# Optimization experiments

Measured on AMD Instinct MI355X. Metric: run time of the kernel, lower is better.

Reference implementation:

```python
import jax, jax.numpy as jnp
import numpy as np

N_NODES = 100000


def _sage_conv(x, edge_index, W_n, W_s, b):
    # edge_index: [2, E] with row0 = src, row1 = dst (messages flow src -> dst)
    src, dst = edge_index[0], edge_index[1]
    msgs = x[src]                                   # [E, F] gather
    summed = jax.ops.segment_sum(msgs, dst, num_segments=N_NODES)   # [N, F]
    deg = jax.ops.segment_sum(jnp.ones((edge_index.shape[1],), x.dtype), dst,
                              num_segments=N_NODES)                 # [N]
    mean = summed / jnp.maximum(deg, 1.0)[:, None]  # mean aggregation
    return mean @ W_n + x @ W_s + b


def setup_inputs() -> dict:
    key = jax.random.key(0)
    ks = jax.random.split(key, 8)
    in_dim, hid_dim, out_dim = 64, 64, 32
    n_edges = 1600000
    x = jax.random.normal(ks[0], (N_NODES, in_dim), dtype=jnp.float32)
    edge_index = jax.random.randint(ks[1], (2, n_edges), 0, N_NODES, dtype=jnp.int64)
    s1 = 1.0 / np.sqrt(in_dim)
    s2 = 1.0 / np.sqrt(hid_dim)
    W1_n = jax.random.uniform(ks[2], (in_dim, hid_dim), jnp.float32, -s1, s1)
    W1_s = jax.random.uniform(ks[3], (in_dim, hid_dim), jnp.float32, -s1, s1)
    b1 = jnp.zeros((hid_dim,), jnp.float32)
    W2_n = jax.random.uniform(ks[4], (hid_dim, out_dim), jnp.float32, -s2, s2)
    W2_s = jax.random.uniform(ks[5], (hid_dim, out_dim), jnp.float32, -s2, s2)
    b2 = jnp.zeros((out_dim,), jnp.float32)
    return {"x": x, "edge_index": edge_index, "W1_n": W1_n, "W1_s": W1_s,
            "b1": b1, "W2_n": W2_n, "W2_s": W2_s, "b2": b2}


def reference(x, edge_index, W1_n, W1_s, b1, W2_n, W2_s, b2):
    h = _sage_conv(x, edge_index, W1_n, W1_s, b1)
    h = jax.nn.relu(h)
    # dropout(p=0.5) is identity in eval mode
    out = _sage_conv(h, edge_index, W2_n, W2_s, b2)
    return out
```

## Files before the change

### kernel.cpp

```cpp
#include <hip/hip_runtime.h>
#include <hip/hip_bf16.h>

#define N_NODES 100000
#define NB 784
#define NPAD 100352
#define BSH 7
#define BMASK 127
#define CAP 4096
#define MSTRIDE 36

typedef float v2f __attribute__((ext_vector_type(2)));

__device__ inline void fma4(float a, const float4& w, float4& c) {
  c.x = fmaf(a, w.x, c.x);
  c.y = fmaf(a, w.y, c.y);
  c.z = fmaf(a, w.z, c.z);
  c.w = fmaf(a, w.w, c.w);
}
__device__ inline unsigned short f2bf(float f) {
  unsigned u = __float_as_uint(f);
  u += 0x7fffu + ((u >> 16) & 1u);
  return (unsigned short)(u >> 16);
}
__device__ inline unsigned pack2bf(float a, float b) {
  return (unsigned)f2bf(a) | ((unsigned)f2bf(b) << 16);
}
__device__ inline unsigned packfp8x4(float a, float b, float c, float d) {
  int pk = __builtin_amdgcn_cvt_pk_fp8_f32(a, b, 0, false);
  pk = __builtin_amdgcn_cvt_pk_fp8_f32(c, d, pk, true);
  return (unsigned)pk;
}
__device__ inline float4 relu_mix(uint2 m, uint2 s) {
  float4 v;
  v.x = fmaxf(__uint_as_float(m.x << 16) + __uint_as_float(s.x << 16), 0.f);
  v.y = fmaxf(__uint_as_float(m.x & 0xffff0000u) +
                  __uint_as_float(s.x & 0xffff0000u), 0.f);
  v.z = fmaxf(__uint_as_float(m.y << 16) + __uint_as_float(s.y << 16), 0.f);
  v.w = fmaxf(__uint_as_float(m.y & 0xffff0000u) +
                  __uint_as_float(s.y & 0xffff0000u), 0.f);
  return v;
}
__device__ inline void acc16(const uint4& u, float* acc) {
  v2f f0 = __builtin_amdgcn_cvt_pk_f32_fp8((int)u.x, false);
  v2f f1 = __builtin_amdgcn_cvt_pk_f32_fp8((int)u.x, true);
  v2f f2 = __builtin_amdgcn_cvt_pk_f32_fp8((int)u.y, false);
  v2f f3 = __builtin_amdgcn_cvt_pk_f32_fp8((int)u.y, true);
  v2f f4 = __builtin_amdgcn_cvt_pk_f32_fp8((int)u.z, false);
  v2f f5 = __builtin_amdgcn_cvt_pk_f32_fp8((int)u.z, true);
  v2f f6 = __builtin_amdgcn_cvt_pk_f32_fp8((int)u.w, false);
  v2f f7 = __builtin_amdgcn_cvt_pk_f32_fp8((int)u.w, true);
  acc[0] += f0[0];  acc[1] += f0[1];
  acc[2] += f1[0];  acc[3] += f1[1];
  acc[4] += f2[0];  acc[5] += f2[1];
  acc[6] += f3[0];  acc[7] += f3[1];
  acc[8] += f4[0];  acc[9] += f4[1];
  acc[10] += f5[0]; acc[11] += f5[1];
  acc[12] += f6[0]; acc[13] += f6[1];
  acc[14] += f7[0]; acc[15] += f7[1];
}

#define EPB 8192
#define EPT 32
#define GB1 1563

__global__ __launch_bounds__(256) void fusedA_k(
    const int* __restrict__ src, const int* __restrict__ dst,
    unsigned* __restrict__ bcur, unsigned* __restrict__ ep,
    const float* __restrict__ x, const float* __restrict__ W1n,
    const float* __restrict__ W1s, const float* __restrict__ b1,
    unsigned* __restrict__ xnb8, unsigned short* __restrict__ xsb,
    int E, int NSB, int M) {
  __shared__ __align__(16) float smem[8192];
  const int tid = threadIdx.x;

  if ((int)blockIdx.x < NSB) {
    unsigned* lh = (unsigned*)smem;
    unsigned* lbase = lh + NB;
    for (int i = tid; i < NB; i += 256) lh[i] = 0;
    __syncthreads();
    const int ebase = blockIdx.x * EPB;
    unsigned rb[EPT];
#pragma unroll
    for (int it = 0; it < EPT; ++it) {
      int e = ebase + it * 256 + tid;
      if (e < E) {
        unsigned b = ((unsigned)dst[e]) >> BSH;
        unsigned r = atomicAdd(&lh[b], 1u);
        rb[it] = (r << 10) | b;
      }
    }
    __syncthreads();
    for (int i = tid; i < NB; i += 256)
      lbase[i] = lh[i] ? atomicAdd(&bcur[i], lh[i]) : 0u;
    __syncthreads();
#pragma unroll
    for (int it = 0; it < EPT; ++it) {
      int e = ebase + it * 256 + tid;
      if (e < E) {
        unsigned b = rb[it] & 1023u;
        unsigned r = rb[it] >> 10;
        ep[(size_t)b * CAP + lbase[b] + r] =
            (((unsigned)src[e]) << BSH) | (((unsigned)dst[e]) & BMASK);
      }
    }
    return;
  }

  float* Wn = smem;
  float* Ws = smem + 4096;
  const int row0 = ((int)blockIdx.x - NSB) * 64;

  for (int i = tid; i < 1024; i += 256) {
    ((float4*)Wn)[i] = ((const float4*)W1n)[i];
    ((float4*)Ws)[i] = ((const float4*)W1s)[i];
  }

  const int tx = tid & 15;
  const int ty = tid >> 4;
  const int arow = ty * 4;

  const float* xr[4];
#pragma unroll
  for (int r = 0; r < 4; ++r) {
    long long gr = row0 + arow + r;
    if (gr >= M) gr = M - 1;
    xr[r] = x + gr * 64;
  }

  float4 an[4], as[4];
#pragma unroll
  for (int r = 0; r < 4; ++r) {
    an[r] = make_float4(0.f, 0.f, 0.f, 0.f);
    as[r] = make_float4(0.f, 0.f, 0.f, 0.f);
  }
  __syncthreads();

#pragma unroll 2
  for (int k4 = 0; k4 < 16; ++k4) {
    float4 a[4];
#pragma unroll
    for (int r = 0; r < 4; ++r) a[r] = *(const float4*)(xr[r] + 4 * k4);
    float4 wn0 = *(const float4*)&Wn[(4 * k4 + 0) * 64 + 4 * tx];
    float4 wn1 = *(const float4*)&Wn[(4 * k4 + 1) * 64 + 4 * tx];
    float4 wn2 = *(const float4*)&Wn[(4 * k4 + 2) * 64 + 4 * tx];
    float4 wn3 = *(const float4*)&Wn[(4 * k4 + 3) * 64 + 4 * tx];
    float4 ws0 = *(const float4*)&Ws[(4 * k4 + 0) * 64 + 4 * tx];
    float4 ws1 = *(const float4*)&Ws[(4 * k4 + 1) * 64 + 4 * tx];
    float4 ws2 = *(const float4*)&Ws[(4 * k4 + 2) * 64 + 4 * tx];
    float4 ws3 = *(const float4*)&Ws[(4 * k4 + 3) * 64 + 4 * tx];
#pragma unroll
    for (int r = 0; r < 4; ++r) {
      fma4(a[r].x, wn0, an[r]);
      fma4(a[r].y, wn1, an[r]);
      fma4(a[r].z, wn2, an[r]);
      fma4(a[r].w, wn3, an[r]);
      fma4(a[r].x, ws0, as[r]);
      fma4(a[r].y, ws1, as[r]);
      fma4(a[r].z, ws2, as[r]);
      fma4(a[r].w, ws3, as[r]);
    }
  }

  const float4 bv = *(const float4*)&b1[4 * tx];
#pragma unroll
  for (int r = 0; r < 4; ++r) {
    int row = row0 + arow + r;
    if (row < M) {
      ushort4 ps;
      ps.x = f2bf(as[r].x + bv.x);
      ps.y = f2bf(as[r].y + bv.y);
      ps.z = f2bf(as[r].z + bv.z);
      ps.w = f2bf(as[r].w + bv.w);
      *(ushort4*)&xsb[(long long)row * 64 + 4 * tx] = ps;
      xnb8[(size_t)row * 16 + tx] =
          packfp8x4(an[r].x, an[r].y, an[r].z, an[r].w);
    }
  }
}

__global__ __launch_bounds__(256) void bsort_k(const unsigned* __restrict__ ep,
                                               const unsigned* __restrict__ bcur,
                                               int* __restrict__ ssrc,
                                               uint2* __restrict__ rows2) {
  __shared__ unsigned cnt[128];
  __shared__ unsigned sc[128];
  const int tid = threadIdx.x;
  const int b = blockIdx.x;
  const unsigned cntb = bcur[b];
  const unsigned beg = (unsigned)(b * CAP);
  if (tid < 128) cnt[tid] = 0;
  __syncthreads();
  for (unsigned j = tid; j < cntb; j += 256)
    atomicAdd(&cnt[ep[(size_t)beg + j] & BMASK], 1u);
  __syncthreads();
  unsigned v = (tid < 128) ? cnt[tid] : 0u;
  if (tid < 128) sc[tid] = v;
  __syncthreads();
  for (int off = 1; off < 128; off <<= 1) {
    unsigned t = (tid < 128 && tid >= off) ? sc[tid - off] : 0u;
    __syncthreads();
    if (tid < 128) sc[tid] += t;
    __syncthreads();
  }
  if (tid < 128) {
    unsigned ex = sc[tid] - v;
    rows2[b * 128 + tid] = make_uint2(beg + ex, beg + ex + v);
    cnt[tid] = ex;
  }
  __syncthreads();
  for (unsigned j = tid; j < cntb; j += 256) {
    unsigned p = ep[(size_t)beg + j];
    unsigned r = atomicAdd(&cnt[p & BMASK], 1u);
    ssrc[(size_t)beg + r] = (int)(p >> BSH);
  }
}

__global__ __launch_bounds__(256) void fgg_k(
    const uint4* __restrict__ valb4, const int* __restrict__ ssrc,
    const uint2* __restrict__ rows2, const unsigned short* __restrict__ xsb,
    const float* __restrict__ W2n, const float* __restrict__ W2s,
    const float* __restrict__ b2, unsigned* __restrict__ hnb8,
    float* __restrict__ hs, int M) {
  __shared__ float Wn[64 * 32];
  __shared__ float Ws[64 * 32];
  __shared__ unsigned mlds[64 * MSTRIDE];
  __shared__ unsigned degs[64];
  __shared__ unsigned begs[64];
  __shared__ unsigned char perm[64];
  const int tid = threadIdx.x;
  const int node0 = blockIdx.x * 64;

  for (int i = tid; i < 512; i += 256) {
    ((float4*)Wn)[i] = ((const float4*)W2n)[i];
    ((float4*)Ws)[i] = ((const float4*)W2s)[i];
  }

  if (tid < 64) {
    uint2 be = rows2[node0 + tid];
    degs[tid] = be.y - be.x;
    begs[tid] = be.x;
  }
  __syncthreads();
  if (tid < 64) {
    unsigned d = degs[tid];
    int rank = 0;
    for (int j2 = 0; j2 < 64; ++j2) {
      unsigned dj = degs[j2];
      rank += (dj < d) || (dj == d && j2 < tid);
    }
    perm[rank] = (unsigned char)tid;
  }
  __syncthreads();

  const int slot = tid >> 2;
  const int lrow = perm[slot];
  const int p = tid & 3;
  const unsigned dg = degs[lrow];
  const unsigned beg = begs[lrow];
  const unsigned end = beg + dg;

  float acc[16];
#pragma unroll
  for (int q = 0; q < 16; ++q) acc[q] = 0.f;

  unsigned j = beg;
  for (; j + 8 <= end; j += 8) {
    int sn[8];
#pragma unroll
    for (int i = 0; i < 8; ++i) sn[i] = ssrc[j + i];
    uint4 u[8];
#pragma unroll
    for (int i = 0; i < 8; ++i) u[i] = valb4[(size_t)sn[i] * 4 + p];
#pragma unroll
    for (int i = 0; i < 8; ++i) acc16(u[i], acc);
  }
  if (j < end) {
    uint4 u[8];
#pragma unroll
    for (int i = 0; i < 8; ++i) {
      u[i] = make_uint4(0u, 0u, 0u, 0u);
      if (j + i < end) {
        int s = ssrc[j + i];
        u[i] = valb4[(size_t)s * 4 + p];
      }
    }
#pragma unroll
    for (int i = 0; i < 8; ++i) acc16(u[i], acc);
  }

  const float inv = dg ? 1.f / (float)dg : 0.f;
  uint4 pk0, pk1;
  pk0.x = pack2bf(acc[0] * inv, acc[1] * inv);
  pk0.y = pack2bf(acc[2] * inv, acc[3] * inv);
  pk0.z = pack2bf(acc[4] * inv, acc[5] * inv);
  pk0.w = pack2bf(acc[6] * inv, acc[7] * inv);
  pk1.x = pack2bf(acc[8] * inv, acc[9] * inv);
  pk1.y = pack2bf(acc[10] * inv, acc[11] * inv);
  pk1.z = pack2bf(acc[12] * inv, acc[13] * inv);
  pk1.w = pack2bf(acc[14] * inv, acc[15] * inv);
  *(uint4*)&mlds[lrow * MSTRIDE + p * 8] = pk0;
  *(uint4*)&mlds[lrow * MSTRIDE + p * 8 + 4] = pk1;
  __syncthreads();

  const int tx = tid & 7;
  const int ty = tid >> 3;
  const int arow = ty * 2;

  const uint2* mp[2];
  const uint2* sp[2];
#pragma unroll
  for (int r = 0; r < 2; ++r) {
    long long gr = node0 + arow + r;
    if (gr >= M) gr = M - 1;
    mp[r] = (const uint2*)&mlds[(arow + r) * MSTRIDE];
    sp[r] = (const uint2*)(xsb + gr * 64);
  }

  float4 an[2], as[2];
#pragma unroll
  for (int r = 0; r < 2; ++r) {
    an[r] = make_float4(0.f, 0.f, 0.f, 0.f);
    as[r] = make_float4(0.f, 0.f, 0.f, 0.f);
  }

#pragma unroll 2
  for (int k4 = 0; k4 < 16; ++k4) {
    float4 a[2];
#pragma unroll
    for (int r = 0; r < 2; ++r) a[r] = relu_mix(mp[r][k4], sp[r][k4]);
    float4 wn0 = *(const float4*)&Wn[(4 * k4 + 0) * 32 + 4 * tx];
    float4 wn1 = *(const float4*)&Wn[(4 * k4 + 1) * 32 + 4 * tx];
    float4 wn2 = *(const float4*)&Wn[(4 * k4 + 2) * 32 + 4 * tx];
    float4 wn3 = *(const float4*)&Wn[(4 * k4 + 3) * 32 + 4 * tx];
    float4 ws0 = *(const float4*)&Ws[(4 * k4 + 0) * 32 + 4 * tx];
    float4 ws1 = *(const float4*)&Ws[(4 * k4 + 1) * 32 + 4 * tx];
    float4 ws2 = *(const float4*)&Ws[(4 * k4 + 2) * 32 + 4 * tx];
    float4 ws3 = *(const float4*)&Ws[(4 * k4 + 3) * 32 + 4 * tx];
#pragma unroll
    for (int r = 0; r < 2; ++r) {
      fma4(a[r].x, wn0, an[r]);
      fma4(a[r].y, wn1, an[r]);
      fma4(a[r].z, wn2, an[r]);
      fma4(a[r].w, wn3, an[r]);
      fma4(a[r].x, ws0, as[r]);
      fma4(a[r].y, ws1, as[r]);
      fma4(a[r].z, ws2, as[r]);
      fma4(a[r].w, ws3, as[r]);
    }
  }

  const float4 bv = *(const float4*)&b2[4 * tx];
#pragma unroll
  for (int r = 0; r < 2; ++r) {
    int row = node0 + arow + r;
    if (row < M) {
      float4 o;
      o.x = as[r].x + bv.x;
      o.y = as[r].y + bv.y;
      o.z = as[r].z + bv.z;
      o.w = as[r].w + bv.w;
      *(float4*)&hs[(long long)row * 32 + 4 * tx] = o;
      hnb8[(size_t)row * 8 + tx] =
          packfp8x4(an[r].x, an[r].y, an[r].z, an[r].w);
    }
  }
}

__global__ __launch_bounds__(256) void gather2_k(
    const uint4* __restrict__ valb4, const int* __restrict__ ssrc,
    const uint2* __restrict__ rows2, const float* __restrict__ base,
    float* __restrict__ out, int N) {
  __shared__ unsigned degs[128];
  __shared__ unsigned begs[128];
  __shared__ unsigned char perm[128];
  const int tid = threadIdx.x;
  const int node0 = blockIdx.x * 128;

  if (tid < 128) {
    uint2 be = rows2[node0 + tid];
    degs[tid] = be.y - be.x;
    begs[tid] = be.x;
  }
  __syncthreads();
  if (tid < 128) {
    unsigned d = degs[tid];
    int rank = 0;
    for (int j2 = 0; j2 < 128; ++j2) {
      unsigned dj = degs[j2];
      rank += (dj < d) || (dj == d && j2 < tid);
    }
    perm[rank] = (unsigned char)tid;
  }
  __syncthreads();

  const int slot = tid >> 1;
  const int lrow = perm[slot];
  const int node = node0 + lrow;
  const int p = tid & 1;
  const unsigned dg = degs[lrow];
  const unsigned beg = begs[lrow];
  const unsigned end = beg + dg;

  float acc[16];
#pragma unroll
  for (int q = 0; q < 16; ++q) acc[q] = 0.f;

  unsigned j = beg;
  for (; j + 8 <= end; j += 8) {
    int sn[8];
#pragma unroll
    for (int i = 0; i < 8; ++i) sn[i] = ssrc[j + i];
    uint4 u[8];
#pragma unroll
    for (int i = 0; i < 8; ++i) u[i] = valb4[(size_t)sn[i] * 2 + p];
#pragma unroll
    for (int i = 0; i < 8; ++i) acc16(u[i], acc);
  }
  if (j < end) {
    uint4 u[8];
#pragma unroll
    for (int i = 0; i < 8; ++i) {
      u[i] = make_uint4(0u, 0u, 0u, 0u);
      if (j + i < end) {
        int s = ssrc[j + i];
        u[i] = valb4[(size_t)s * 2 + p];
      }
    }
#pragma unroll
    for (int i = 0; i < 8; ++i) acc16(u[i], acc);
  }

  if (node < N) {
    const float inv = dg ? 1.f / (float)dg : 0.f;
    const size_t o = (size_t)node * 32 + 16 * p;
#pragma unroll
    for (int q4 = 0; q4 < 4; ++q4) {
      float4 bv = *(const float4*)&base[o + 4 * q4];
      float4 ov;
      ov.x = acc[4 * q4 + 0] * inv + bv.x;
      ov.y = acc[4 * q4 + 1] * inv + bv.y;
      ov.z = acc[4 * q4 + 2] * inv + bv.z;
      ov.w = acc[4 * q4 + 3] * inv + bv.w;
      *(float4*)&out[o + 4 * q4] = ov;
    }
  }
}

extern "C" void kernel_launch(void* const* d_in, const int* in_sizes, int n_in,
                              void* d_out, int out_size, void* d_ws,
                              size_t ws_size, hipStream_t stream) {
  const float* x   = (const float*)d_in[0];
  const int*   ei  = (const int*)d_in[1];
  const float* W1n = (const float*)d_in[2];
  const float* W1s = (const float*)d_in[3];
  const float* b1  = (const float*)d_in[4];
  const float* W2n = (const float*)d_in[5];
  const float* W2s = (const float*)d_in[6];
  const float* b2  = (const float*)d_in[7];
  float* out = (float*)d_out;

  const int E = in_sizes[1] / 2;
  const int M = N_NODES;
  const int* src = ei;
  const int* dst = ei + E;
  const int NSB = (E + EPB - 1) / EPB;

  char* wsb = (char*)d_ws;
  unsigned*       ep    = (unsigned*)(wsb);
  int*            ssrc  = (int*)(wsb + 12845056);
  uint2*          rows2 = (uint2*)(wsb + 25690112);
  unsigned*       bcur  = (unsigned*)(wsb + 26492928);
  unsigned*       xnb8  = (unsigned*)(wsb + 26496064);
  unsigned short* xsb   = (unsigned short*)(wsb + 32896064);
  float*          hs    = (float*)(wsb + 45696064);
  unsigned*       hnb8  = (unsigned*)(wsb);

  hipMemsetAsync(bcur, 0, NB * 4, stream);
  fusedA_k<<<NSB + GB1, 256, 0, stream>>>(src, dst, bcur, ep, x, W1n, W1s, b1,
                                          xnb8, xsb, E, NSB, M);
  bsort_k<<<NB, 256, 0, stream>>>(ep, bcur, ssrc, rows2);
  fgg_k<<<GB1, 256, 0, stream>>>((const uint4*)xnb8, ssrc, rows2, xsb, W2n,
                                 W2s, b2, hnb8, hs, M);
  gather2_k<<<(M + 127) / 128, 256, 0, stream>>>((const uint4*)hnb8, ssrc,
                                                 rows2, hs, out, M);
}
```

Before: 216.1 us.

## Split each node's edge range across two threads and drop degree sorting

In both gather kernels, each node's neighbor list is now split in half and given to two threads, whose partial sums are combined with a cross-lane shuffle. This replaces the in-block degree ranking and permutation, which added shared memory, two barriers and O(n^2) rank work. The edge tail now uses clamped unconditional loads with a 0/1 weight instead of branches. Blocks cover fewer nodes (32 in fgg, 64 in gather2), so more blocks run. Without degree sorting, lanes in a wavefront may see more divergence when neighboring nodes have different degrees.

```diff
diff --git a/kernel.cpp b/kernel.cpp
--- a/kernel.cpp
+++ b/kernel.cpp
@@ -8,6 +8,7 @@
 #define BMASK 127
 #define CAP 4096
 #define MSTRIDE 36
+#define FNB 32
 
 typedef float v2f __attribute__((ext_vector_type(2)));
 
@@ -58,6 +59,24 @@
   acc[12] += f6[0]; acc[13] += f6[1];
   acc[14] += f7[0]; acc[15] += f7[1];
 }
+__device__ inline void macc16(const uint4& u, float w, float* acc) {
+  v2f f0 = __builtin_amdgcn_cvt_pk_f32_fp8((int)u.x, false);
+  v2f f1 = __builtin_amdgcn_cvt_pk_f32_fp8((int)u.x, true);
+  v2f f2 = __builtin_amdgcn_cvt_pk_f32_fp8((int)u.y, false);
+  v2f f3 = __builtin_amdgcn_cvt_pk_f32_fp8((int)u.y, true);
+  v2f f4 = __builtin_amdgcn_cvt_pk_f32_fp8((int)u.z, false);
+  v2f f5 = __builtin_amdgcn_cvt_pk_f32_fp8((int)u.z, true);
+  v2f f6 = __builtin_amdgcn_cvt_pk_f32_fp8((int)u.w, false);
+  v2f f7 = __builtin_amdgcn_cvt_pk_f32_fp8((int)u.w, true);
+  acc[0] = fmaf(w, f0[0], acc[0]);   acc[1] = fmaf(w, f0[1], acc[1]);
+  acc[2] = fmaf(w, f1[0], acc[2]);   acc[3] = fmaf(w, f1[1], acc[3]);
+  acc[4] = fmaf(w, f2[0], acc[4]);   acc[5] = fmaf(w, f2[1], acc[5]);
+  acc[6] = fmaf(w, f3[0], acc[6]);   acc[7] = fmaf(w, f3[1], acc[7]);
+  acc[8] = fmaf(w, f4[0], acc[8]);   acc[9] = fmaf(w, f4[1], acc[9]);
+  acc[10] = fmaf(w, f5[0], acc[10]); acc[11] = fmaf(w, f5[1], acc[11]);
+  acc[12] = fmaf(w, f6[0], acc[12]); acc[13] = fmaf(w, f6[1], acc[13]);
+  acc[14] = fmaf(w, f7[0], acc[14]); acc[15] = fmaf(w, f7[1], acc[15]);
+}
 
 #define EPB 8192
 #define EPT 32
@@ -223,48 +242,32 @@
     float* __restrict__ hs, int M) {
   __shared__ float Wn[64 * 32];
   __shared__ float Ws[64 * 32];
-  __shared__ unsigned mlds[64 * MSTRIDE];
-  __shared__ unsigned degs[64];
-  __shared__ unsigned begs[64];
-  __shared__ unsigned char perm[64];
+  __shared__ unsigned mlds[FNB * MSTRIDE];
   const int tid = threadIdx.x;
-  const int node0 = blockIdx.x * 64;
+  const int node0 = blockIdx.x * FNB;
 
   for (int i = tid; i < 512; i += 256) {
     ((float4*)Wn)[i] = ((const float4*)W2n)[i];
     ((float4*)Ws)[i] = ((const float4*)W2s)[i];
   }
 
-  if (tid < 64) {
-    uint2 be = rows2[node0 + tid];
-    degs[tid] = be.y - be.x;
-    begs[tid] = be.x;
-  }
-  __syncthreads();
-  if (tid < 64) {
-    unsigned d = degs[tid];
-    int rank = 0;
-    for (int j2 = 0; j2 < 64; ++j2) {
-      unsigned dj = degs[j2];
-      rank += (dj < d) || (dj == d && j2 < tid);
-    }
-    perm[rank] = (unsigned char)tid;
-  }
-  __syncthreads();
-
-  const int slot = tid >> 2;
-  const int lrow = perm[slot];
-  const int p = tid & 3;
-  const unsigned dg = degs[lrow];
-  const unsigned beg = begs[lrow];
-  const unsigned end = beg + dg;
+  const int lrow = tid >> 3;
+  const int q = tid & 7;
+  const int p = q & 3;
+  const int t = q >> 2;
+  const int node = node0 + lrow;
+  const uint2 be = rows2[node];
+  const unsigned dg = be.y - be.x;
+  const unsigned mid = be.x + ((dg + 1) >> 1);
+  const unsigned tb = t ? mid : be.x;
+  const unsigned te = t ? be.y : mid;
 
   float acc[16];
 #pragma unroll
-  for (int q = 0; q < 16; ++q) acc[q] = 0.f;
-
-  unsigned j = beg;
-  for (; j + 8 <= end; j += 8) {
+  for (int qq = 0; qq < 16; ++qq) acc[qq] = 0.f;
+
+  unsigned j = tb;
+  for (; j + 8 <= te; j += 8) {
     int sn[8];
 #pragma unroll
     for (int i = 0; i < 8; ++i) sn[i] = ssrc[j + i];
@@ -274,60 +277,53 @@
 #pragma unroll
     for (int i = 0; i < 8; ++i) acc16(u[i], acc);
   }
-  if (j < end) {
+  if (j < te) {
+    const unsigned last = te - 1;
+    int sn[8];
+#pragma unroll
+    for (int i = 0; i < 8; ++i) {
+      unsigned jj = j + i;
+      sn[i] = ssrc[jj < last ? jj : last];
+    }
     uint4 u[8];
 #pragma unroll
-    for (int i = 0; i < 8; ++i) {
-      u[i] = make_uint4(0u, 0u, 0u, 0u);
-      if (j + i < end) {
-        int s = ssrc[j + i];
-        u[i] = valb4[(size_t)s * 4 + p];
-      }
-    }
-#pragma unroll
-    for (int i = 0; i < 8; ++i) acc16(u[i], acc);
-  }
+    for (int i = 0; i < 8; ++i) u[i] = valb4[(size_t)sn[i] * 4 + p];
+#pragma unroll
+    for (int i = 0; i < 8; ++i) macc16(u[i], ((j + i) < te) ? 1.f : 0.f, acc);
+  }
+
+#pragma unroll
+  for (int qq = 0; qq < 16; ++qq) acc[qq] += __shfl_xor(acc[qq], 4);
 
   const float inv = dg ? 1.f / (float)dg : 0.f;
-  uint4 pk0, pk1;
-  pk0.x = pack2bf(acc[0] * inv, acc[1] * inv);
-  pk0.y = pack2bf(acc[2] * inv, acc[3] * inv);
-  pk0.z = pack2bf(acc[4] * inv, acc[5] * inv);
-  pk0.w = pack2bf(acc[6] * inv, acc[7] * inv);
-  pk1.x = pack2bf(acc[8] * inv, acc[9] * inv);
-  pk1.y = pack2bf(acc[10] * inv, acc[11] * inv);
-  pk1.z = pack2bf(acc[12] * inv, acc[13] * inv);
-  pk1.w = pack2bf(acc[14] * inv, acc[15] * inv);
-  *(uint4*)&mlds[lrow * MSTRIDE + p * 8] = pk0;
-  *(uint4*)&mlds[lrow * MSTRIDE + p * 8 + 4] = pk1;
+  if (t == 0) {
+    uint4 pk;
+    pk.x = pack2bf(acc[0] * inv, acc[1] * inv);
+    pk.y = pack2bf(acc[2] * inv, acc[3] * inv);
+    pk.z = pack2bf(acc[4] * inv, acc[5] * inv);
+    pk.w = pack2bf(acc[6] * inv, acc[7] * inv);
+    *(uint4*)&mlds[lrow * MSTRIDE + p * 8] = pk;
+  } else {
+    uint4 pk;
+    pk.x = pack2bf(acc[8] * inv, acc[9] * inv);
+    pk.y = pack2bf(acc[10] * inv, acc[11] * inv);
+    pk.z = pack2bf(acc[12] * inv, acc[13] * inv);
+    pk.w = pack2bf(acc[14] * inv, acc[15] * inv);
+    *(uint4*)&mlds[lrow * MSTRIDE + p * 8 + 4] = pk;
+  }
   __syncthreads();
 
   const int tx = tid & 7;
   const int ty = tid >> 3;
-  const int arow = ty * 2;
-
-  const uint2* mp[2];
-  const uint2* sp[2];
-#pragma unroll
-  for (int r = 0; r < 2; ++r) {
-    long long gr = node0 + arow + r;
-    if (gr >= M) gr = M - 1;
-    mp[r] = (const uint2*)&mlds[(arow + r) * MSTRIDE];
-    sp[r] = (const uint2*)(xsb + gr * 64);
-  }
-
-  float4 an[2], as[2];
-#pragma unroll
-  for (int r = 0; r < 2; ++r) {
-    an[r] = make_float4(0.f, 0.f, 0.f, 0.f);
-    as[r] = make_float4(0.f, 0.f, 0.f, 0.f);
-  }
+  const uint2* mp = (const uint2*)&mlds[ty * MSTRIDE];
+  const uint2* sp = (const uint2*)(xsb + (long long)(node0 + ty) * 64);
+
+  float4 an = make_float4(0.f, 0.f, 0.f, 0.f);
+  float4 asv = make_float4(0.f, 0.f, 0.f, 0.f);
 
 #pragma unroll 2
   for (int k4 = 0; k4 < 16; ++k4) {
-    float4 a[2];
-#pragma unroll
-    for (int r = 0; r < 2; ++r) a[r] = relu_mix(mp[r][k4], sp[r][k4]);
+    float4 a = relu_mix(mp[k4], sp[k4]);
     float4 wn0 = *(const float4*)&Wn[(4 * k4 + 0) * 32 + 4 * tx];
     float4 wn1 = *(const float4*)&Wn[(4 * k4 + 1) * 32 + 4 * tx];
     float4 wn2 = *(const float4*)&Wn[(4 * k4 + 2) * 32 + 4 * tx];
@@ -336,77 +332,50 @@
     float4 ws1 = *(const float4*)&Ws[(4 * k4 + 1) * 32 + 4 * tx];
     float4 ws2 = *(const float4*)&Ws[(4 * k4 + 2) * 32 + 4 * tx];
     float4 ws3 = *(const float4*)&Ws[(4 * k4 + 3) * 32 + 4 * tx];
-#pragma unroll
-    for (int r = 0; r < 2; ++r) {
-      fma4(a[r].x, wn0, an[r]);
-      fma4(a[r].y, wn1, an[r]);
-      fma4(a[r].z, wn2, an[r]);
-      fma4(a[r].w, wn3, an[r]);
-      fma4(a[r].x, ws0, as[r]);
-      fma4(a[r].y, ws1, as[r]);
-      fma4(a[r].z, ws2, as[r]);
-      fma4(a[r].w, ws3, as[r]);
-    }
+    fma4(a.x, wn0, an);
+    fma4(a.y, wn1, an);
+    fma4(a.z, wn2, an);
+    fma4(a.w, wn3, an);
+    fma4(a.x, ws0, asv);
+    fma4(a.y, ws1, asv);
+    fma4(a.z, ws2, asv);
+    fma4(a.w, ws3, asv);
   }
 
   const float4 bv = *(const float4*)&b2[4 * tx];
-#pragma unroll
-  for (int r = 0; r < 2; ++r) {
-    int row = node0 + arow + r;
-    if (row < M) {
-      float4 o;
-      o.x = as[r].x + bv.x;
-      o.y = as[r].y + bv.y;
-      o.z = as[r].z + bv.z;
-      o.w = as[r].w + bv.w;
-      *(float4*)&hs[(long long)row * 32 + 4 * tx] = o;
-      hnb8[(size_t)row * 8 + tx] =
-          packfp8x4(an[r].x, an[r].y, an[r].z, an[r].w);
-    }
-  }
+  const int row = node0 + ty;
+  float4 o;
+  o.x = asv.x + bv.x;
+  o.y = asv.y + bv.y;
+  o.z = asv.z + bv.z;
+  o.w = asv.w + bv.w;
+  *(float4*)&hs[(long long)row * 32 + 4 * tx] = o;
+  hnb8[(size_t)row * 8 + tx] = packfp8x4(an.x, an.y, an.z, an.w);
 }
 
 __global__ __launch_bounds__(256) void gather2_k(
     const uint4* __restrict__ valb4, const int* __restrict__ ssrc,
     const uint2* __restrict__ rows2, const float* __restrict__ base,
     float* __restrict__ out, int N) {
-  __shared__ unsigned degs[128];
-  __shared__ unsigned begs[128];
-  __shared__ unsigned char perm[128];
   const int tid = threadIdx.x;
-  const int node0 = blockIdx.x * 128;
-
-  if (tid < 128) {
-    uint2 be = rows2[node0 + tid];
-    degs[tid] = be.y - be.x;
-    begs[tid] = be.x;
-  }
-  __syncthreads();
-  if (tid < 128) {
-    unsigned d = degs[tid];
-    int rank = 0;
-    for (int j2 = 0; j2 < 128; ++j2) {
-      unsigned dj = degs[j2];
-      rank += (dj < d) || (dj == d && j2 < tid);
-    }
-    perm[rank] = (unsigned char)tid;
-  }
-  __syncthreads();
-
-  const int slot = tid >> 1;
-  const int lrow = perm[slot];
+  const int node0 = blockIdx.x * 64;
+  const int lrow = tid >> 2;
+  const int q = tid & 3;
+  const int p = q & 1;
+  const int t = q >> 1;
   const int node = node0 + lrow;
-  const int p = tid & 1;
-  const unsigned dg = degs[lrow];
-  const unsigned beg = begs[lrow];
-  const unsigned end = beg + dg;
+  const uint2 be = rows2[node];
+  const unsigned dg = be.y - be.x;
+  const unsigned mid = be.x + ((dg + 1) >> 1);
+  const unsigned tb = t ? mid : be.x;
+  const unsigned te = t ? be.y : mid;
 
   float acc[16];
 #pragma unroll
-  for (int q = 0; q < 16; ++q) acc[q] = 0.f;
-
-  unsigned j = beg;
-  for (; j + 8 <= end; j += 8) {
+  for (int qq = 0; qq < 16; ++qq) acc[qq] = 0.f;
+
+  unsigned j = tb;
+  for (; j + 8 <= te; j += 8) {
     int sn[8];
 #pragma unroll
     for (int i = 0; i < 8; ++i) sn[i] = ssrc[j + i];
@@ -416,25 +385,30 @@
 #pragma unroll
     for (int i = 0; i < 8; ++i) acc16(u[i], acc);
   }
-  if (j < end) {
+  if (j < te) {
+    const unsigned last = te - 1;
+    int sn[8];
+#pragma unroll
+    for (int i = 0; i < 8; ++i) {
+      unsigned jj = j + i;
+      sn[i] = ssrc[jj < last ? jj : last];
+    }
     uint4 u[8];
 #pragma unroll
-    for (int i = 0; i < 8; ++i) {
-      u[i] = make_uint4(0u, 0u, 0u, 0u);
-      if (j + i < end) {
-        int s = ssrc[j + i];
-        u[i] = valb4[(size_t)s * 2 + p];
-      }
-    }
-#pragma unroll
-    for (int i = 0; i < 8; ++i) acc16(u[i], acc);
-  }
+    for (int i = 0; i < 8; ++i) u[i] = valb4[(size_t)sn[i] * 2 + p];
+#pragma unroll
+    for (int i = 0; i < 8; ++i) macc16(u[i], ((j + i) < te) ? 1.f : 0.f, acc);
+  }
+
+#pragma unroll
+  for (int qq = 0; qq < 16; ++qq) acc[qq] += __shfl_xor(acc[qq], 2);
 
   if (node < N) {
     const float inv = dg ? 1.f / (float)dg : 0.f;
     const size_t o = (size_t)node * 32 + 16 * p;
 #pragma unroll
-    for (int q4 = 0; q4 < 4; ++q4) {
+    for (int h = 0; h < 2; ++h) {
+      const int q4 = 2 * t + h;
       float4 bv = *(const float4*)&base[o + 4 * q4];
       float4 ov;
       ov.x = acc[4 * q4 + 0] * inv + bv.x;
@@ -479,8 +453,9 @@
   fusedA_k<<<NSB + GB1, 256, 0, stream>>>(src, dst, bcur, ep, x, W1n, W1s, b1,
                                           xnb8, xsb, E, NSB, M);
   bsort_k<<<NB, 256, 0, stream>>>(ep, bcur, ssrc, rows2);
-  fgg_k<<<GB1, 256, 0, stream>>>((const uint4*)xnb8, ssrc, rows2, xsb, W2n,
-                                 W2s, b2, hnb8, hs, M);
-  gather2_k<<<(M + 127) / 128, 256, 0, stream>>>((const uint4*)hnb8, ssrc,
-                                                 rows2, hs, out, M);
-}
+  fgg_k<<<(M + FNB - 1) / FNB, 256, 0, stream>>>((const uint4*)xnb8, ssrc,
+                                                 rows2, xsb, W2n, W2s, b2,
+                                                 hnb8, hs, M);
+  gather2_k<<<(M + 63) / 64, 256, 0, stream>>>((const uint4*)hnb8, ssrc,
+                                               rows2, hs, out, M);
+}
```

After: 194.6 us. 9.9% less time.
